# Kernel tuning notes

Hardware: AMD Instinct MI355X
Metric: run time of the kernel (lower is better)

The kernel has to match this reference:

```python
import jax, jax.numpy as jnp
import numpy as np

VOCAB = 32000
EMB = 512
HEADS = 8
HEAD_DIM = EMB // HEADS
MLP = 2048
LAYERS = 6
KERNEL_EPS = 1e-3  # performer generalized-attention kernel_epsilon
LN_EPS = 1e-6


def sinusoidal_pos_emb(seq_len, dim):
    pos = np.arange(seq_len)[:, None].astype(np.float32)
    div = np.exp(np.arange(0, dim, 2).astype(np.float32) * (-np.log(10000.0) / dim))
    pe = np.zeros((seq_len, dim), dtype=np.float32)
    pe[:, 0::2] = np.sin(pos * div)
    pe[:, 1::2] = np.cos(pos * div)
    return jnp.asarray(pe)


def setup_inputs() -> dict:
    key = jax.random.key(0)
    ks = jax.random.split(key, 16)
    B, S = 4, 4096
    s_emb = 1.0 / np.sqrt(EMB)
    s_head = 1.0 / np.sqrt(HEAD_DIM)
    s_mlp = 1.0 / np.sqrt(MLP)
    return {
        'tokens': jax.random.randint(ks[0], (B, S), 0, VOCAB),
        'embed': jax.random.normal(ks[1], (VOCAB, EMB), jnp.float32) * s_emb,
        'Wq': jax.random.normal(ks[2], (LAYERS, EMB, HEADS, HEAD_DIM), jnp.float32) * s_emb,
        'Wk': jax.random.normal(ks[3], (LAYERS, EMB, HEADS, HEAD_DIM), jnp.float32) * s_emb,
        'Wv': jax.random.normal(ks[4], (LAYERS, EMB, HEADS, HEAD_DIM), jnp.float32) * s_emb,
        'Wo': jax.random.normal(ks[5], (LAYERS, HEADS, HEAD_DIM, EMB), jnp.float32) * s_head,
        'ln1_s': jnp.ones((LAYERS, EMB), jnp.float32),
        'ln1_b': jnp.zeros((LAYERS, EMB), jnp.float32),
        'W1': jax.random.normal(ks[6], (LAYERS, EMB, MLP), jnp.float32) * s_emb,
        'b1': jnp.zeros((LAYERS, MLP), jnp.float32),
        'W2': jax.random.normal(ks[7], (LAYERS, MLP, EMB), jnp.float32) * s_mlp,
        'b2': jnp.zeros((LAYERS, EMB), jnp.float32),
        'ln2_s': jnp.ones((LAYERS, EMB), jnp.float32),
        'ln2_b': jnp.zeros((LAYERS, EMB), jnp.float32),
        'lnf_s': jnp.ones((EMB,), jnp.float32),
        'lnf_b': jnp.zeros((EMB,), jnp.float32),
    }


def layer_norm(x, s, b):
    mu = jnp.mean(x, axis=-1, keepdims=True)
    var = jnp.mean(jnp.square(x - mu), axis=-1, keepdims=True)
    return (x - mu) * jax.lax.rsqrt(var + LN_EPS) * s + b


def favor_generalized_attention(x, Wq, Wk, Wv, Wo):
    # Performer generalized attention, deterministic ReLU feature map,
    # renormalized (bidirectional): O(S * m * d) linear attention.
    q = jnp.einsum('bsd,dhf->bshf', x, Wq)
    k = jnp.einsum('bsd,dhf->bshf', x, Wk)
    v = jnp.einsum('bsd,dhf->bshf', x, Wv)
    pq = jax.nn.relu(q) + KERNEL_EPS  # phi(q): [B,S,H,F]
    pk = jax.nn.relu(k) + KERNEL_EPS  # phi(k)
    kv = jnp.einsum('bshf,bshe->bhfe', pk, v)          # [B,H,F,E]
    num = jnp.einsum('bshf,bhfe->bshe', pq, kv)        # numerator
    den = jnp.einsum('bshf,bhf->bsh', pq, pk.sum(axis=1))  # renormalizer
    attn = num / den[..., None]
    return jnp.einsum('bshe,hed->bsd', attn, Wo)


def reference(tokens, embed, Wq, Wk, Wv, Wo, ln1_s, ln1_b, W1, b1, W2, b2,
              ln2_s, ln2_b, lnf_s, lnf_b):
    B, S = tokens.shape
    x = embed[tokens] + sinusoidal_pos_emb(S, EMB)[None, :, :]
    for l in range(LAYERS):
        h = layer_norm(x, ln1_s[l], ln1_b[l])
        x = x + favor_generalized_attention(h, Wq[l], Wk[l], Wv[l], Wo[l])
        h = layer_norm(x, ln2_s[l], ln2_b[l])
        h = jax.nn.gelu(h @ W1[l] + b1[l]) @ W2[l] + b2[l]
        x = x + h
    return layer_norm(x, lnf_s, lnf_b)
```

## Files before the change

### kernel.cpp

```cpp
#include <hip/hip_runtime.h>

typedef float f32x4 __attribute__((ext_vector_type(4)));
typedef __bf16 bf16x8 __attribute__((ext_vector_type(8)));

#define NROWS 16384
#define SEQ   4096
#define EMBD  512
#define MLPD  2048

__device__ inline float gelu_tanh(float x) {
    float t = 0.7978845608028654f * (x + 0.044715f * x * x * x);
    float e = __expf(2.f * t);
    float th = 1.f - 2.f / (1.f + e);
    return 0.5f * x * (1.f + th);
}

#define GLOAD16(gp, lp)                                                        \
    __builtin_amdgcn_global_load_lds(                                          \
        (const __attribute__((address_space(1))) void*)(gp),                   \
        (__attribute__((address_space(3))) void*)(lp), 16, 0, 0)

__global__ void pos_kernel(float* __restrict__ pos) {
    int i = blockIdx.x * 256 + threadIdx.x;
    int s = i >> 8, j = i & 255;
    float div = __expf((float)j * (-2.f * 9.210340371976184f / 512.f));
    float a = (float)s * div;
    pos[(size_t)s * 512 + 2 * j]     = sinf(a);
    pos[(size_t)s * 512 + 2 * j + 1] = cosf(a);
}

__global__ __launch_bounds__(256) void embed_ln(
    const int* __restrict__ tokens, const float* __restrict__ embed,
    const float* __restrict__ pos, const float* __restrict__ gamma,
    const float* __restrict__ beta, float* __restrict__ x,
    __bf16* __restrict__ h) {
    int lane = threadIdx.x & 63;
    size_t row = (size_t)blockIdx.x * 4 + (threadIdx.x >> 6);
    int s = (int)(row & (SEQ - 1));
    int tok = tokens[row];
    const float* ep = embed + (size_t)tok * 512 + lane * 8;
    const float* pp = pos + (size_t)s * 512 + lane * 8;
    f32x4 v0 = *(const f32x4*)ep + *(const f32x4*)pp;
    f32x4 v1 = *(const f32x4*)(ep + 4) + *(const f32x4*)(pp + 4);
    *(f32x4*)(x + row * 512 + lane * 8) = v0;
    *(f32x4*)(x + row * 512 + lane * 8 + 4) = v1;
    float sum = (v0[0] + v0[1]) + (v0[2] + v0[3]) + (v1[0] + v1[1]) + (v1[2] + v1[3]);
    #pragma unroll
    for (int off = 32; off; off >>= 1) sum += __shfl_xor(sum, off);
    float mu = sum * (1.f / 512.f);
    float vs = 0.f;
    #pragma unroll
    for (int j = 0; j < 4; j++) {
        float d0 = v0[j] - mu; vs += d0 * d0;
        float d1 = v1[j] - mu; vs += d1 * d1;
    }
    #pragma unroll
    for (int off = 32; off; off >>= 1) vs += __shfl_xor(vs, off);
    float inv = rsqrtf(vs * (1.f / 512.f) + 1e-6f);
    const float* gp = gamma + lane * 8;
    const float* bp = beta + lane * 8;
    f32x4 g0 = *(const f32x4*)gp, g1 = *(const f32x4*)(gp + 4);
    f32x4 bb0 = *(const f32x4*)bp, bb1 = *(const f32x4*)(bp + 4);
    bf16x8 ov;
    #pragma unroll
    for (int j = 0; j < 4; j++) {
        ov[j]     = (__bf16)((v0[j] - mu) * inv * g0[j] + bb0[j]);
        ov[4 + j] = (__bf16)((v1[j] - mu) * inv * g1[j] + bb1[j]);
    }
    *(bf16x8*)(h + row * 512 + lane * 8) = ov;
}

__global__ void transpose_bf16(const float* __restrict__ in, __bf16* __restrict__ out,
                               int K, int N, size_t in_lstride, size_t out_lstride) {
    __shared__ float tile[32][33];
    in  += (size_t)blockIdx.z * in_lstride;
    out += (size_t)blockIdx.z * out_lstride;
    int n0 = blockIdx.x * 32, k0 = blockIdx.y * 32;
    int tx = threadIdx.x, ty = threadIdx.y;
    #pragma unroll
    for (int i = 0; i < 32; i += 8)
        tile[ty + i][tx] = in[(size_t)(k0 + ty + i) * N + n0 + tx];
    __syncthreads();
    #pragma unroll
    for (int i = 0; i < 32; i += 8)
        out[(size_t)(n0 + ty + i) * K + k0 + tx] = (__bf16)tile[tx][ty + i];
}

template<int EPI, int K>
__global__ __launch_bounds__(512, 4) void gemm_bt(
    const __bf16* __restrict__ A, const __bf16* __restrict__ BT,
    __bf16* __restrict__ Cb, const float* __restrict__ bias, int N, int nbn) {
    constexpr int NT = K / 32;
    __shared__ __align__(16) __bf16 smem[3 * (256 + 128) * 32];
    __bf16* Asm0 = smem;
    __bf16* Bsm0 = smem + 3 * 256 * 32;
    const int t = threadIdx.x;
    const int lane = t & 63;
    const int wave = t >> 6;
    const int wr = wave >> 1, wc = wave & 1;
    const int nblk = gridDim.x;
    const int q = nblk >> 3, r = nblk & 7;
    const int xcd = blockIdx.x & 7, loc = blockIdx.x >> 3;
    const int swz = (xcd < r ? xcd * (q + 1) : r * (q + 1) + (xcd - r) * q) + loc;
    const int m0 = (swz / nbn) * 256, n0 = (swz % nbn) * 128;
    const int fr = lane & 15, fc = lane >> 4;

    const __bf16* Aps[2];
    int aslot[2];
    #pragma unroll
    for (int j = 0; j < 2; j++) {
        int slot = t + 512 * j;
        int row = slot >> 2, cp = slot & 3;
        int sc = cp ^ ((row >> 1) & 3);
        Aps[j] = A + (size_t)(m0 + row) * K + sc * 8;
        aslot[j] = slot * 8;
    }
    const __bf16* Bp;
    int bslot;
    {
        int row = t >> 2, cp = t & 3;
        int sc = cp ^ ((row >> 1) & 3);
        Bp = BT + (size_t)(n0 + row) * K + sc * 8;
        bslot = t * 8;
    }

    f32x4 acc[4][4];
    #pragma unroll
    for (int m = 0; m < 4; m++)
        #pragma unroll
        for (int n = 0; n < 4; n++)
            acc[m][n] = (f32x4){0.f, 0.f, 0.f, 0.f};

    auto stage = [&](int koff, __bf16* Ad, __bf16* Bd) {
        GLOAD16(Aps[0] + koff, Ad + aslot[0]);
        GLOAD16(Aps[1] + koff, Ad + aslot[1]);
        GLOAD16(Bp + koff, Bd + bslot);
    };

    stage(0, Asm0, Bsm0);
    stage(32, Asm0 + 256 * 32, Bsm0 + 128 * 32);

    for (int s = 0; s < NT; s++) {
        if (s + 1 < NT) {
            asm volatile("s_waitcnt vmcnt(3)" ::: "memory");
        } else {
            asm volatile("s_waitcnt vmcnt(0)" ::: "memory");
        }
        __builtin_amdgcn_s_barrier();
        if (s + 2 < NT) {
            int sl = (s + 2) % 3;
            stage((s + 2) * 32, Asm0 + sl * 256 * 32, Bsm0 + sl * 128 * 32);
        }
        const __bf16* Ac = Asm0 + (s % 3) * 256 * 32;
        const __bf16* Bc = Bsm0 + (s % 3) * 128 * 32;

        bf16x8 af[4], bfr[4];
        #pragma unroll
        for (int m = 0; m < 4; m++) {
            int ra = wr * 64 + m * 16 + fr;
            af[m] = *(const bf16x8*)(Ac + ra * 32 + ((fc ^ ((ra >> 1) & 3)) << 3));
        }
        #pragma unroll
        for (int n = 0; n < 4; n++) {
            int rb = wc * 64 + n * 16 + fr;
            bfr[n] = *(const bf16x8*)(Bc + rb * 32 + ((fc ^ ((rb >> 1) & 3)) << 3));
        }
        __builtin_amdgcn_s_setprio(1);
        #pragma unroll
        for (int m = 0; m < 4; m++)
            #pragma unroll
            for (int n = 0; n < 4; n++)
                acc[m][n] = __builtin_amdgcn_mfma_f32_16x16x32_bf16(af[m], bfr[n], acc[m][n], 0, 0, 0);
        __builtin_amdgcn_s_setprio(0);
    }

    const int cr = (lane >> 4) * 4;
    const int cc = lane & 15;
    __bf16* Cs = smem;
    __syncthreads();
    #pragma unroll
    for (int m = 0; m < 4; m++) {
        #pragma unroll
        for (int n = 0; n < 4; n++) {
            #pragma unroll
            for (int r2 = 0; r2 < 4; r2++) {
                int lrow = wr * 64 + m * 16 + cr + r2;
                int lcol = wc * 64 + n * 16 + cc;
                float val = acc[m][n][r2];
                if (EPI == 1) {
                    if (n0 + lcol < 1024) val = fmaxf(val, 0.f) + 1e-3f;
                } else {
                    val = gelu_tanh(val + bias[n0 + lcol]);
                }
                Cs[lrow * 136 + lcol] = (__bf16)val;
            }
        }
    }
    __syncthreads();
    for (int i = t; i < 256 * 16; i += 512) {
        int row = i >> 4, c8 = i & 15;
        bf16x8 v = *(const bf16x8*)(Cs + row * 136 + c8 * 8);
        *(bf16x8*)(Cb + (size_t)(m0 + row) * N + n0 + c8 * 8) = v;
    }
}

template<int HASB, int K, int FINAL>
__global__ __launch_bounds__(1024) void gemm_ln(
    const __bf16* __restrict__ A, const __bf16* __restrict__ BT,
    const float* __restrict__ bias, float* __restrict__ x,
    const float* __restrict__ gamma, const float* __restrict__ beta,
    __bf16* __restrict__ hout, float* __restrict__ fout) {
    constexpr int NT = K / 64;
    __shared__ __align__(16) __bf16 smem[2 * 64 * 64 + 2 * 512 * 64];
    __shared__ float sums[64][8][2];
    __shared__ float rowstat[64][2];
    __bf16* Aring = smem;
    __bf16* Bring = smem + 2 * 64 * 64;
    const int t = threadIdx.x;
    const int lane = t & 63;
    const int wave = t >> 6;
    const int wr = wave >> 3;
    const int wc = wave & 7;
    const int m0 = blockIdx.x * 64;
    const int fr = lane & 15, fc = lane >> 4;

    const __bf16* Ap = A;
    int aslot = 0;
    if (t < 512) {
        int row = t >> 3, cp = t & 7;
        int sc = cp ^ (row & 7);
        Ap = A + (size_t)(m0 + row) * K + sc * 8;
        aslot = t * 8;
    }
    const __bf16* Bps[4];
    int bslot[4];
    #pragma unroll
    for (int j = 0; j < 4; j++) {
        int slot = t + 1024 * j;
        int row = slot >> 3, cp = slot & 7;
        int sc = cp ^ (row & 7);
        Bps[j] = BT + (size_t)row * K + sc * 8;
        bslot[j] = slot * 8;
    }
    auto stage = [&](int ss) {
        int sl = ss & 1;
        #pragma unroll
        for (int j = 0; j < 4; j++) GLOAD16(Bps[j] + ss * 64, Bring + sl * 32768 + bslot[j]);
        if (t < 512) GLOAD16(Ap + ss * 64, Aring + sl * 4096 + aslot);
    };

    f32x4 acc[2][4];
    #pragma unroll
    for (int m = 0; m < 2; m++)
        #pragma unroll
        for (int n = 0; n < 4; n++)
            acc[m][n] = (f32x4){0.f, 0.f, 0.f, 0.f};

    stage(0);
    for (int s = 0; s < NT; s++) {
        asm volatile("s_waitcnt vmcnt(0)" ::: "memory");
        __builtin_amdgcn_s_barrier();
        if (s + 1 < NT) stage(s + 1);
        const __bf16* Ac = Aring + (s & 1) * 4096;
        const __bf16* Bc = Bring + (s & 1) * 32768;
        #pragma unroll
        for (int kk = 0; kk < 2; kk++) {
            bf16x8 af[2], bfr[4];
            #pragma unroll
            for (int m = 0; m < 2; m++) {
                int ra = wr * 32 + m * 16 + fr;
                int c = kk * 4 + fc;
                af[m] = *(const bf16x8*)(Ac + ra * 64 + ((c ^ (ra & 7)) << 3));
            }
            #pragma unroll
            for (int n = 0; n < 4; n++) {
                int rb = wc * 64 + n * 16 + fr;
                int c = kk * 4 + fc;
                bfr[n] = *(const bf16x8*)(Bc + rb * 64 + ((c ^ (rb & 7)) << 3));
            }
            __builtin_amdgcn_s_setprio(1);
            #pragma unroll
            for (int m = 0; m < 2; m++)
                #pragma unroll
                for (int n = 0; n < 4; n++)
                    acc[m][n] = __builtin_amdgcn_mfma_f32_16x16x32_bf16(af[m], bfr[n], acc[m][n], 0, 0, 0);
            __builtin_amdgcn_s_setprio(0);
        }
    }

    const int cr = (lane >> 4) * 4;
    const int cc = lane & 15;
    float bia[4], gam[4], bet[4];
    #pragma unroll
    for (int n = 0; n < 4; n++) {
        int gcol = wc * 64 + n * 16 + cc;
        bia[n] = HASB ? bias[gcol] : 0.f;
        gam[n] = gamma[gcol];
        bet[n] = beta[gcol];
    }
    float xn[2][4][4];
    #pragma unroll
    for (int m = 0; m < 2; m++) {
        #pragma unroll
        for (int r2 = 0; r2 < 4; r2++) {
            int grow = m0 + wr * 32 + m * 16 + cr + r2;
            #pragma unroll
            for (int n = 0; n < 4; n++) {
                int gcol = wc * 64 + n * 16 + cc;
                xn[m][n][r2] = acc[m][n][r2] + bia[n] + x[(size_t)grow * 512 + gcol];
            }
        }
    }
    #pragma unroll
    for (int m = 0; m < 2; m++) {
        #pragma unroll
        for (int r2 = 0; r2 < 4; r2++) {
            float s1 = 0.f, q1 = 0.f;
            #pragma unroll
            for (int n = 0; n < 4; n++) { float v = xn[m][n][r2]; s1 += v; q1 += v * v; }
            #pragma unroll
            for (int off = 1; off <= 8; off <<= 1) {
                s1 += __shfl_xor(s1, off);
                q1 += __shfl_xor(q1, off);
            }
            if (cc == 0) {
                int rl = wr * 32 + m * 16 + cr + r2;
                sums[rl][wc][0] = s1;
                sums[rl][wc][1] = q1;
            }
        }
    }
    __syncthreads();
    if (t < 64) {
        float S = 0.f, Q = 0.f;
        #pragma unroll
        for (int w = 0; w < 8; w++) { S += sums[t][w][0]; Q += sums[t][w][1]; }
        float mu = S * (1.f / 512.f);
        float var = Q * (1.f / 512.f) - mu * mu;
        rowstat[t][0] = mu;
        rowstat[t][1] = rsqrtf(var + 1e-6f);
    }
    __syncthreads();
    __bf16* Hs = smem;
    #pragma unroll
    for (int m = 0; m < 2; m++) {
        #pragma unroll
        for (int r2 = 0; r2 < 4; r2++) {
            int rl = wr * 32 + m * 16 + cr + r2;
            int grow = m0 + rl;
            float mu = rowstat[rl][0], inv = rowstat[rl][1];
            #pragma unroll
            for (int n = 0; n < 4; n++) {
                int gcol = wc * 64 + n * 16 + cc;
                float v = xn[m][n][r2];
                float hv = (v - mu) * inv * gam[n] + bet[n];
                if (!FINAL) {
                    x[(size_t)grow * 512 + gcol] = v;
                    Hs[rl * 520 + gcol] = (__bf16)hv;
                } else {
                    fout[(size_t)grow * 512 + gcol] = hv;
                }
            }
        }
    }
    if (!FINAL) {
        __syncthreads();
        for (int i = t; i < 64 * 64; i += 1024) {
            int row = i >> 6, c8 = i & 63;
            bf16x8 v = *(const bf16x8*)(Hs + row * 520 + c8 * 8);
            *(bf16x8*)(hout + (size_t)(m0 + row) * 512 + c8 * 8) = v;
        }
    }
}

__global__ __launch_bounds__(256) void kv_partial(const __bf16* __restrict__ qkvb,
                                                  float* __restrict__ part) {
    int bh = blockIdx.x;
    int chunk = blockIdx.y;
    int b = bh >> 3, hh = bh & 7;
    int t = threadIdx.x;
    int f = t & 63, eg = t >> 6;
    size_t base = ((size_t)b * SEQ + (size_t)chunk * 64) * 1536;
    const __bf16* kcol = qkvb + base + 512 + hh * 64 + f;
    const __bf16* vrow = qkvb + base + 1024 + hh * 64 + eg * 16;
    float psum = 0.f;
    f32x4 a0 = {0.f,0.f,0.f,0.f}, a1 = a0, a2 = a0, a3 = a0;
    for (int s = 0; s < 64; s++) {
        size_t o = (size_t)s * 1536;
        float pk = (float)kcol[o];
        psum += pk;
        bf16x8 w0 = *(const bf16x8*)(vrow + o);
        bf16x8 w1 = *(const bf16x8*)(vrow + o + 8);
        #pragma unroll
        for (int j = 0; j < 4; j++) {
            a0[j] += (float)w0[j]     * pk;
            a1[j] += (float)w0[4 + j] * pk;
            a2[j] += (float)w1[j]     * pk;
            a3[j] += (float)w1[4 + j] * pk;
        }
    }
    float* dst = part + ((size_t)chunk * 32 + bh) * 4160 + (size_t)f * 65 + eg * 16;
    #pragma unroll
    for (int j = 0; j < 4; j++) { dst[j] = a0[j]; dst[4+j] = a1[j]; dst[8+j] = a2[j]; dst[12+j] = a3[j]; }
    if (eg == 0) dst[64] = psum;
}

__global__ void kv_reduce(const float* __restrict__ part, float* __restrict__ kvfin) {
    int i = blockIdx.x * 256 + threadIdx.x;
    if (i >= 32 * 4160) return;
    float s = 0.f;
    #pragma unroll 8
    for (int c = 0; c < 64; c++) s += part[(size_t)c * (32 * 4160) + i];
    kvfin[i] = s;
}

__global__ __launch_bounds__(256) void num_attn(const __bf16* __restrict__ qkvb,
                                                const float* __restrict__ kvfin,
                                                __bf16* __restrict__ attn) {
    __shared__ __bf16 kvb[64][86];
    __shared__ __bf16 cs[128][72];
    int bh = blockIdx.x, chunk = blockIdx.y;
    int b = bh >> 3, hh = bh & 7;
    const float* src = kvfin + (size_t)bh * 4160;
    int t = threadIdx.x;
    for (int i = t; i < 4096; i += 256) {
        int f = i >> 6, e = i & 63;
        kvb[f][e] = (__bf16)src[f * 65 + e];
    }
    if (t < 64) {
        kvb[t][64] = (__bf16)src[t * 65 + 64];
        #pragma unroll
        for (int e = 65; e < 80; e++) kvb[t][e] = (__bf16)0.f;
    }
    const int lane = t & 63, w = t >> 6;
    const int fr = lane & 15, fc = lane >> 4;
    size_t rowbase = (size_t)b * SEQ + (size_t)chunk * 128 + w * 32;
    bf16x8 a[2][2];
    #pragma unroll
    for (int rt = 0; rt < 2; rt++)
        #pragma unroll
        for (int ks = 0; ks < 2; ks++)
            a[rt][ks] = *(const bf16x8*)(qkvb + (rowbase + rt * 16 + fr) * 1536 + hh * 64 + ks * 32 + fc * 8);
    __syncthreads();
    bf16x8 bfrag[5][2];
    #pragma unroll
    for (int n = 0; n < 5; n++)
        #pragma unroll
        for (int ks = 0; ks < 2; ks++) {
            bf16x8 bv;
            #pragma unroll
            for (int j = 0; j < 8; j++) bv[j] = kvb[ks * 32 + fc * 8 + j][n * 16 + fr];
            bfrag[n][ks] = bv;
        }
    f32x4 acc[2][5];
    #pragma unroll
    for (int rt = 0; rt < 2; rt++)
        #pragma unroll
        for (int n = 0; n < 5; n++)
            acc[rt][n] = (f32x4){0.f, 0.f, 0.f, 0.f};
    #pragma unroll
    for (int ks = 0; ks < 2; ks++)
        #pragma unroll
        for (int rt = 0; rt < 2; rt++)
            #pragma unroll
            for (int n = 0; n < 5; n++)
                acc[rt][n] = __builtin_amdgcn_mfma_f32_16x16x32_bf16(a[rt][ks], bfrag[n][ks], acc[rt][n], 0, 0, 0);
    const int cr = (lane >> 4) * 4, cc = lane & 15;
    #pragma unroll
    for (int rt = 0; rt < 2; rt++) {
        float rdv[4];
        #pragma unroll
        for (int r2 = 0; r2 < 4; r2++)
            rdv[r2] = 1.f / __shfl(acc[rt][4][r2], lane & 48);
        #pragma unroll
        for (int r2 = 0; r2 < 4; r2++) {
            int lr = w * 32 + rt * 16 + cr + r2;
            #pragma unroll
            for (int n = 0; n < 4; n++)
                cs[lr][n * 16 + cc] = (__bf16)(acc[rt][n][r2] * rdv[r2]);
        }
    }
    __syncthreads();
    size_t base = (size_t)b * SEQ + (size_t)chunk * 128;
    for (int i = t; i < 128 * 8; i += 256) {
        int row = i >> 3, c8 = i & 7;
        bf16x8 v = *(const bf16x8*)(&cs[row][c8 * 8]);
        *(bf16x8*)(attn + (base + row) * 512 + hh * 64 + c8 * 8) = v;
    }
}

extern "C" void kernel_launch(void* const* d_in, const int* in_sizes, int n_in,
                              void* d_out, int out_size, void* d_ws, size_t ws_size,
                              hipStream_t stream) {
    const int*   tokens = (const int*)d_in[0];
    const float* embed  = (const float*)d_in[1];
    const float* Wq     = (const float*)d_in[2];
    const float* Wk     = (const float*)d_in[3];
    const float* Wv     = (const float*)d_in[4];
    const float* Wo     = (const float*)d_in[5];
    const float* ln1_s  = (const float*)d_in[6];
    const float* ln1_b  = (const float*)d_in[7];
    const float* W1     = (const float*)d_in[8];
    const float* b1     = (const float*)d_in[9];
    const float* W2     = (const float*)d_in[10];
    const float* b2     = (const float*)d_in[11];
    const float* ln2_s  = (const float*)d_in[12];
    const float* ln2_b  = (const float*)d_in[13];
    const float* lnf_s  = (const float*)d_in[14];
    const float* lnf_b  = (const float*)d_in[15];
    float* out = (float*)d_out;

    float* ws = (float*)d_ws;
    size_t off = 0;
    float* pos = ws;               off += 2097152;
    float* x   = ws + off;         off += 8388608;
    __bf16* h    = (__bf16*)(ws + off); off += 4194304;
    __bf16* attn = (__bf16*)(ws + off); off += 4194304;
    __bf16* qkvb = (__bf16*)(ws + off);
    __bf16* hid  = (__bf16*)(ws + off); off += 16777216;
    float* kvpart = ws + off;      off += 64 * 32 * 4160;
    float* kvfin  = ws + off;      off += 32 * 4160;
    __bf16* wbuf  = (__bf16*)(ws + off);

    pos_kernel<<<4096, 256, 0, stream>>>(pos);
    transpose_bf16<<<dim3(16, 16, 6), dim3(32, 8), 0, stream>>>(Wq, wbuf,          512, 512,  262144, 3145728);
    transpose_bf16<<<dim3(16, 16, 6), dim3(32, 8), 0, stream>>>(Wk, wbuf + 262144, 512, 512,  262144, 3145728);
    transpose_bf16<<<dim3(16, 16, 6), dim3(32, 8), 0, stream>>>(Wv, wbuf + 524288, 512, 512,  262144, 3145728);
    transpose_bf16<<<dim3(16, 16, 6), dim3(32, 8), 0, stream>>>(Wo, wbuf + 786432, 512, 512,  262144, 3145728);
    transpose_bf16<<<dim3(64, 16, 6), dim3(32, 8), 0, stream>>>(W1, wbuf + 1048576, 512, 2048, 1048576, 3145728);
    transpose_bf16<<<dim3(16, 64, 6), dim3(32, 8), 0, stream>>>(W2, wbuf + 2097152, 2048, 512, 1048576, 3145728);
    embed_ln<<<4096, 256, 0, stream>>>(tokens, embed, pos, ln1_s, ln1_b, x, h);

    for (int l = 0; l < 6; l++) {
        const __bf16* wl = wbuf + (size_t)l * 3145728;
        gemm_bt<1, 512><<<768, 512, 0, stream>>>(h, wl, qkvb, nullptr, 1536, 12);
        kv_partial<<<dim3(32, 64), 256, 0, stream>>>(qkvb, kvpart);
        kv_reduce<<<520, 256, 0, stream>>>(kvpart, kvfin);
        num_attn<<<dim3(32, 32), 256, 0, stream>>>(qkvb, kvfin, attn);
        gemm_ln<0, 512, 0><<<256, 1024, 0, stream>>>(attn, wl + 786432, nullptr, x,
                                                     ln2_s + l * 512, ln2_b + l * 512, h, nullptr);
        gemm_bt<3, 512><<<1024, 512, 0, stream>>>(h, wl + 1048576, hid, b1 + (size_t)l * 2048, 2048, 16);
        if (l < 5) {
            gemm_ln<1, 2048, 0><<<256, 1024, 0, stream>>>(hid, wl + 2097152, b2 + (size_t)l * 512, x,
                                                          ln1_s + (l + 1) * 512, ln1_b + (l + 1) * 512, h, nullptr);
        } else {
            gemm_ln<1, 2048, 1><<<256, 1024, 0, stream>>>(hid, wl + 2097152, b2 + (size_t)l * 512, x,
                                                          lnf_s, lnf_b, nullptr, out);
        }
    }
}
```

Baseline: 1.443 ms.

## Restructure gemm_bt to 1024 threads with K=64 double-buffered LDS tiles

The bf16 GEMM used for the QKV and first MLP projections now runs 16 waves per block instead of 8. Each wave computes a 64x32 sub-tile instead of 64x64, and the K step grows from 32 to 64 with an 8-way XOR swizzle. The 3-stage LDS ring with partial vmcnt waits becomes a 2-stage double buffer that waits for all loads before each barrier. The goal is more waves to hide latency and fewer barriers per tile, but it costs lower per-wave MFMA reuse, higher LDS use per block, and less prefetch overlap.

```diff
diff --git a/kernel.cpp b/kernel.cpp
--- a/kernel.cpp
+++ b/kernel.cpp
@@ -87,17 +87,18 @@
 }
 
 template<int EPI, int K>
-__global__ __launch_bounds__(512, 4) void gemm_bt(
+__global__ __launch_bounds__(1024) void gemm_bt(
     const __bf16* __restrict__ A, const __bf16* __restrict__ BT,
     __bf16* __restrict__ Cb, const float* __restrict__ bias, int N, int nbn) {
-    constexpr int NT = K / 32;
-    __shared__ __align__(16) __bf16 smem[3 * (256 + 128) * 32];
+    constexpr int NT = K / 64;
+    __shared__ __align__(16) __bf16 smem[2 * (256 + 128) * 64];
     __bf16* Asm0 = smem;
-    __bf16* Bsm0 = smem + 3 * 256 * 32;
+    __bf16* Bsm0 = smem + 2 * 256 * 64;
     const int t = threadIdx.x;
     const int lane = t & 63;
     const int wave = t >> 6;
-    const int wr = wave >> 1, wc = wave & 1;
+    const int wr = wave >> 2;
+    const int wc = wave & 3;
     const int nblk = gridDim.x;
     const int q = nblk >> 3, r = nblk & 7;
     const int xcd = blockIdx.x & 7, loc = blockIdx.x >> 3;
@@ -109,26 +110,26 @@
     int aslot[2];
     #pragma unroll
     for (int j = 0; j < 2; j++) {
-        int slot = t + 512 * j;
-        int row = slot >> 2, cp = slot & 3;
-        int sc = cp ^ ((row >> 1) & 3);
+        int slot = t + 1024 * j;
+        int row = slot >> 3, cp = slot & 7;
+        int sc = cp ^ (row & 7);
         Aps[j] = A + (size_t)(m0 + row) * K + sc * 8;
         aslot[j] = slot * 8;
     }
     const __bf16* Bp;
     int bslot;
     {
-        int row = t >> 2, cp = t & 3;
-        int sc = cp ^ ((row >> 1) & 3);
+        int row = t >> 3, cp = t & 7;
+        int sc = cp ^ (row & 7);
         Bp = BT + (size_t)(n0 + row) * K + sc * 8;
         bslot = t * 8;
     }
 
-    f32x4 acc[4][4];
+    f32x4 acc[4][2];
     #pragma unroll
     for (int m = 0; m < 4; m++)
         #pragma unroll
-        for (int n = 0; n < 4; n++)
+        for (int n = 0; n < 2; n++)
             acc[m][n] = (f32x4){0.f, 0.f, 0.f, 0.f};
 
     auto stage = [&](int koff, __bf16* Ad, __bf16* Bd) {
@@ -138,40 +139,36 @@
     };
 
     stage(0, Asm0, Bsm0);
-    stage(32, Asm0 + 256 * 32, Bsm0 + 128 * 32);
-
     for (int s = 0; s < NT; s++) {
-        if (s + 1 < NT) {
-            asm volatile("s_waitcnt vmcnt(3)" ::: "memory");
-        } else {
-            asm volatile("s_waitcnt vmcnt(0)" ::: "memory");
-        }
+        asm volatile("s_waitcnt vmcnt(0)" ::: "memory");
         __builtin_amdgcn_s_barrier();
-        if (s + 2 < NT) {
-            int sl = (s + 2) % 3;
-            stage((s + 2) * 32, Asm0 + sl * 256 * 32, Bsm0 + sl * 128 * 32);
-        }
-        const __bf16* Ac = Asm0 + (s % 3) * 256 * 32;
-        const __bf16* Bc = Bsm0 + (s % 3) * 128 * 32;
-
-        bf16x8 af[4], bfr[4];
-        #pragma unroll
-        for (int m = 0; m < 4; m++) {
-            int ra = wr * 64 + m * 16 + fr;
-            af[m] = *(const bf16x8*)(Ac + ra * 32 + ((fc ^ ((ra >> 1) & 3)) << 3));
-        }
-        #pragma unroll
-        for (int n = 0; n < 4; n++) {
-            int rb = wc * 64 + n * 16 + fr;
-            bfr[n] = *(const bf16x8*)(Bc + rb * 32 + ((fc ^ ((rb >> 1) & 3)) << 3));
-        }
-        __builtin_amdgcn_s_setprio(1);
-        #pragma unroll
-        for (int m = 0; m < 4; m++)
-            #pragma unroll
-            for (int n = 0; n < 4; n++)
-                acc[m][n] = __builtin_amdgcn_mfma_f32_16x16x32_bf16(af[m], bfr[n], acc[m][n], 0, 0, 0);
-        __builtin_amdgcn_s_setprio(0);
+        if (s + 1 < NT)
+            stage((s + 1) * 64, Asm0 + ((s + 1) & 1) * 16384, Bsm0 + ((s + 1) & 1) * 8192);
+        const __bf16* Ac = Asm0 + (s & 1) * 16384;
+        const __bf16* Bc = Bsm0 + (s & 1) * 8192;
+        #pragma unroll
+        for (int kk = 0; kk < 2; kk++) {
+            bf16x8 af[4], bfr[2];
+            #pragma unroll
+            for (int m = 0; m < 4; m++) {
+                int ra = wr * 64 + m * 16 + fr;
+                int c = kk * 4 + fc;
+                af[m] = *(const bf16x8*)(Ac + ra * 64 + ((c ^ (ra & 7)) << 3));
+            }
+            #pragma unroll
+            for (int n = 0; n < 2; n++) {
+                int rb = wc * 32 + n * 16 + fr;
+                int c = kk * 4 + fc;
+                bfr[n] = *(const bf16x8*)(Bc + rb * 64 + ((c ^ (rb & 7)) << 3));
+            }
+            __builtin_amdgcn_s_setprio(1);
+            #pragma unroll
+            for (int m = 0; m < 4; m++)
+                #pragma unroll
+                for (int n = 0; n < 2; n++)
+                    acc[m][n] = __builtin_amdgcn_mfma_f32_16x16x32_bf16(af[m], bfr[n], acc[m][n], 0, 0, 0);
+            __builtin_amdgcn_s_setprio(0);
+        }
     }
 
     const int cr = (lane >> 4) * 4;
@@ -181,11 +178,11 @@
     #pragma unroll
     for (int m = 0; m < 4; m++) {
         #pragma unroll
-        for (int n = 0; n < 4; n++) {
+        for (int n = 0; n < 2; n++) {
             #pragma unroll
             for (int r2 = 0; r2 < 4; r2++) {
                 int lrow = wr * 64 + m * 16 + cr + r2;
-                int lcol = wc * 64 + n * 16 + cc;
+                int lcol = wc * 32 + n * 16 + cc;
                 float val = acc[m][n][r2];
                 if (EPI == 1) {
                     if (n0 + lcol < 1024) val = fmaxf(val, 0.f) + 1e-3f;
@@ -197,7 +194,7 @@
         }
     }
     __syncthreads();
-    for (int i = t; i < 256 * 16; i += 512) {
+    for (int i = t; i < 256 * 16; i += 1024) {
         int row = i >> 4, c8 = i & 15;
         bf16x8 v = *(const bf16x8*)(Cs + row * 136 + c8 * 8);
         *(bf16x8*)(Cb + (size_t)(m0 + row) * N + n0 + c8 * 8) = v;
@@ -533,13 +530,13 @@
 
     for (int l = 0; l < 6; l++) {
         const __bf16* wl = wbuf + (size_t)l * 3145728;
-        gemm_bt<1, 512><<<768, 512, 0, stream>>>(h, wl, qkvb, nullptr, 1536, 12);
+        gemm_bt<1, 512><<<768, 1024, 0, stream>>>(h, wl, qkvb, nullptr, 1536, 12);
         kv_partial<<<dim3(32, 64), 256, 0, stream>>>(qkvb, kvpart);
         kv_reduce<<<520, 256, 0, stream>>>(kvpart, kvfin);
         num_attn<<<dim3(32, 32), 256, 0, stream>>>(qkvb, kvfin, attn);
         gemm_ln<0, 512, 0><<<256, 1024, 0, stream>>>(attn, wl + 786432, nullptr, x,
                                                      ln2_s + l * 512, ln2_b + l * 512, h, nullptr);
-        gemm_bt<3, 512><<<1024, 512, 0, stream>>>(h, wl + 1048576, hid, b1 + (size_t)l * 2048, 2048, 16);
+        gemm_bt<3, 512><<<1024, 1024, 0, stream>>>(h, wl + 1048576, hid, b1 + (size_t)l * 2048, 2048, 16);
         if (l < 5) {
             gemm_ln<1, 2048, 0><<<256, 1024, 0, stream>>>(hid, wl + 2097152, b2 + (size_t)l * 512, x,
                                                           ln1_s + (l + 1) * 512, ln1_b + (l + 1) * 512, h, nullptr);
```

New measurement: 1.512 ms. +4.8%, slower.
